# Performance work log

Measured on AMD Instinct MI355X. Metric: run time of the kernel, lower is better.

The kernel has to match this reference:

```python
import jax, jax.numpy as jnp
import numpy as np

B, L, A, D = 4096, 4096, 4, 128


def setup_inputs() -> dict:
    key = jax.random.key(0)
    ks = jax.random.split(key, 12)
    return {
        "sequence": jax.random.randint(ks[0], (B, L), 0, A, dtype=jnp.int32),
        "baseline_sketch": jax.random.normal(ks[1], (B, D), dtype=jnp.float32),
        # learnable params (match torch init distributions)
        "char_scales": 1.0 + 0.2 * jax.random.normal(ks[2], (A,), dtype=jnp.float32),
        "dimension_weights": 1.0 + 0.3 * jax.random.normal(ks[3], (D,), dtype=jnp.float32),
        "sketch_bias": jnp.zeros((D,), dtype=jnp.float32),
        "char_hash_modifiers": 0.1 * jax.random.normal(ks[4], (A, D), dtype=jnp.float32),
        "W1": jax.random.normal(ks[5], (D, D), dtype=jnp.float32) / np.sqrt(D),
        "b1": jnp.zeros((D,), dtype=jnp.float32),
        "W2": jax.random.normal(ks[6], (D, D), dtype=jnp.float32) / np.sqrt(D),
        "b2": jnp.zeros((D,), dtype=jnp.float32),
    }


def _char_counts(sequence, alphabet_size):
    # Fused histogram over the batch: counts[b, a] = #{t : sequence[b, t] == a, 0 <= a < A}
    b, l = sequence.shape
    valid = (sequence >= 0) & (sequence < alphabet_size)
    # out-of-range chars go to an overflow bucket that is dropped
    ids = jnp.where(valid, sequence, alphabet_size) + (
        jnp.arange(b, dtype=sequence.dtype)[:, None] * (alphabet_size + 1)
    )
    counts = jax.ops.segment_sum(
        jnp.ones((b * l,), dtype=jnp.float32),
        ids.reshape(-1),
        num_segments=b * (alphabet_size + 1),
    ).reshape(b, alphabet_size + 1)[:, :alphabet_size]
    return counts  # [B, A]


def reference(sequence, baseline_sketch, char_scales, dimension_weights,
              sketch_bias, char_hash_modifiers, W1, b1, W2, b2):
    l = sequence.shape[1]
    counts = _char_counts(sequence, char_scales.shape[0])          # [B, A]
    char_probs = counts / l                                        # [B, A]
    scale = char_probs @ char_scales                               # [B]
    # scatter-sum of modifier rows == counts @ modifiers
    mods = (counts @ char_hash_modifiers) / l                      # [B, D]
    e = baseline_sketch * dimension_weights + sketch_bias          # [B, D]
    e = e * scale[:, None] + mods                                  # [B, D]
    h = jax.nn.relu(e @ W1.T + b1)                                 # [B, D]
    return h @ W2.T + b2                                           # [B, D]
```

## Files before the change

kernel.cpp:

```cpp
#include <hip/hip_runtime.h>


static constexpr int Lc = 4096;
static constexpr int Ac = 4;
static constexpr int Dc = 128;

static constexpr int HROWS = 2;

__global__ __launch_bounds__(256, 4)
void hist_kernel(const int* __restrict__ seq, float* __restrict__ counts_out)
{
    const int t    = threadIdx.x;
    const int wave = t >> 6;
    const int lane = t & 63;
    const long long r0 = (long long)blockIdx.x * HROWS;

    __shared__ unsigned long long part[HROWS][4];

    unsigned long long c0 = 0ull, c1 = 0ull;
    {
        const int4* p0 = reinterpret_cast<const int4*>(seq + r0 * Lc);
        const int4* p1 = reinterpret_cast<const int4*>(seq + (r0 + 1) * Lc);
        #pragma unroll
        for (int i = 0; i < Lc / 4 / 256; ++i) {
            const int4 a = p0[i * 256 + t];
            const int4 b = p1[i * 256 + t];
            c0 += 1ull << (((unsigned)a.x & 3u) << 4);
            c0 += 1ull << (((unsigned)a.y & 3u) << 4);
            c0 += 1ull << (((unsigned)a.z & 3u) << 4);
            c0 += 1ull << (((unsigned)a.w & 3u) << 4);
            c1 += 1ull << (((unsigned)b.x & 3u) << 4);
            c1 += 1ull << (((unsigned)b.y & 3u) << 4);
            c1 += 1ull << (((unsigned)b.z & 3u) << 4);
            c1 += 1ull << (((unsigned)b.w & 3u) << 4);
        }
    }
    #pragma unroll
    for (int off = 32; off > 0; off >>= 1) {
        c0 += __shfl_down(c0, off);
        c1 += __shfl_down(c1, off);
    }
    if (lane == 0) { part[0][wave] = c0; part[1][wave] = c1; }
    __syncthreads();

    if (t < HROWS * 4) {
        const int rw = t >> 2, a = t & 3;
        const unsigned long long s =
            part[rw][0] + part[rw][1] + part[rw][2] + part[rw][3];
        counts_out[(r0 + rw) * Dc + a] =
            (float)((unsigned)((s >> (a * 16)) & 0xFFFFull));
    }
}

static constexpr int RPB = 8;

__global__ __launch_bounds__(256, 2)
void mlp_kernel(
    const float* __restrict__ baseline,
    const float* __restrict__ char_scales,
    const float* __restrict__ dim_w,
    const float* __restrict__ sk_bias,
    const float* __restrict__ mods,
    const float* __restrict__ W1,
    const float* __restrict__ b1,
    const float* __restrict__ W2,
    const float* __restrict__ b2,
    float*       __restrict__ out)
{
    __shared__ __align__(16) float e_lds[RPB][Dc];
    __shared__ __align__(16) float h_lds[RPB][Dc];
    __shared__ __align__(16) float psum[8][RPB][Dc];

    const int t    = threadIdx.x;
    const int r0   = blockIdx.x * RPB;
    const int j    = t & (Dc - 1);
    const int half = t >> 7;
    const float invL = 1.0f / (float)Lc;

    {
        const float s0 = char_scales[0], s1 = char_scales[1],
                    s2 = char_scales[2], s3 = char_scales[3];
        const float dwj = dim_w[j], bj = sk_bias[j];
        const float m0 = mods[0 * Dc + j], m1 = mods[1 * Dc + j],
                    m2 = mods[2 * Dc + j], m3 = mods[3 * Dc + j];
        #pragma unroll
        for (int rr = 0; rr < RPB / 2; ++rr) {
            const int r = half + rr * 2;
            const float* cp = out + (long long)(r0 + r) * Dc;
            const float c0 = cp[0], c1 = cp[1], c2 = cp[2], c3 = cp[3];
            const float scale = (c0 * s0 + c1 * s1 + c2 * s2 + c3 * s3) * invL;
            const float md    = (c0 * m0 + c1 * m1 + c2 * m2 + c3 * m3) * invL;
            const float base  = baseline[(long long)(r0 + r) * Dc + j];
            e_lds[r][j] = (base * dwj + bj) * scale + md;
        }
    }
    __syncthreads();

    const int q  = t >> 5;
    const int jg = t & 31;
    const int k0 = q * 16;

    {
        float a0[RPB], a1[RPB], a2[RPB], a3[RPB];
        #pragma unroll
        for (int r = 0; r < RPB; ++r) { a0[r] = 0.f; a1[r] = 0.f; a2[r] = 0.f; a3[r] = 0.f; }
        const float4* w0 = reinterpret_cast<const float4*>(W1 + (jg     ) * Dc + k0);
        const float4* w1 = reinterpret_cast<const float4*>(W1 + (jg + 32) * Dc + k0);
        const float4* w2 = reinterpret_cast<const float4*>(W1 + (jg + 64) * Dc + k0);
        const float4* w3 = reinterpret_cast<const float4*>(W1 + (jg + 96) * Dc + k0);
        #pragma unroll
        for (int kk = 0; kk < 4; ++kk) {
            const float4 wa = w0[kk];
            const float4 wb = w1[kk];
            const float4 wc = w2[kk];
            const float4 wd = w3[kk];
            #pragma unroll
            for (int r = 0; r < RPB; ++r) {
                const float4 e = *reinterpret_cast<const float4*>(&e_lds[r][k0 + kk * 4]);
                a0[r] += wa.x * e.x + wa.y * e.y + wa.z * e.z + wa.w * e.w;
                a1[r] += wb.x * e.x + wb.y * e.y + wb.z * e.z + wb.w * e.w;
                a2[r] += wc.x * e.x + wc.y * e.y + wc.z * e.z + wc.w * e.w;
                a3[r] += wd.x * e.x + wd.y * e.y + wd.z * e.z + wd.w * e.w;
            }
        }
        #pragma unroll
        for (int r = 0; r < RPB; ++r) {
            psum[q][r][jg     ] = a0[r];
            psum[q][r][jg + 32] = a1[r];
            psum[q][r][jg + 64] = a2[r];
            psum[q][r][jg + 96] = a3[r];
        }
    }
    __syncthreads();
    {
        const float b = b1[j];
        #pragma unroll
        for (int rr = 0; rr < RPB / 2; ++rr) {
            const int r = half + rr * 2;
            float s = b;
            #pragma unroll
            for (int qq = 0; qq < 8; ++qq) s += psum[qq][r][j];
            h_lds[r][j] = s > 0.0f ? s : 0.0f;
        }
    }
    __syncthreads();

    {
        float a0[RPB], a1[RPB], a2[RPB], a3[RPB];
        #pragma unroll
        for (int r = 0; r < RPB; ++r) { a0[r] = 0.f; a1[r] = 0.f; a2[r] = 0.f; a3[r] = 0.f; }
        const float4* w0 = reinterpret_cast<const float4*>(W2 + (jg     ) * Dc + k0);
        const float4* w1 = reinterpret_cast<const float4*>(W2 + (jg + 32) * Dc + k0);
        const float4* w2 = reinterpret_cast<const float4*>(W2 + (jg + 64) * Dc + k0);
        const float4* w3 = reinterpret_cast<const float4*>(W2 + (jg + 96) * Dc + k0);
        #pragma unroll
        for (int kk = 0; kk < 4; ++kk) {
            const float4 wa = w0[kk];
            const float4 wb = w1[kk];
            const float4 wc = w2[kk];
            const float4 wd = w3[kk];
            #pragma unroll
            for (int r = 0; r < RPB; ++r) {
                const float4 h = *reinterpret_cast<const float4*>(&h_lds[r][k0 + kk * 4]);
                a0[r] += wa.x * h.x + wa.y * h.y + wa.z * h.z + wa.w * h.w;
                a1[r] += wb.x * h.x + wb.y * h.y + wb.z * h.z + wb.w * h.w;
                a2[r] += wc.x * h.x + wc.y * h.y + wc.z * h.z + wc.w * h.w;
                a3[r] += wd.x * h.x + wd.y * h.y + wd.z * h.z + wd.w * h.w;
            }
        }
        #pragma unroll
        for (int r = 0; r < RPB; ++r) {
            psum[q][r][jg     ] = a0[r];
            psum[q][r][jg + 32] = a1[r];
            psum[q][r][jg + 64] = a2[r];
            psum[q][r][jg + 96] = a3[r];
        }
    }
    __syncthreads();
    {
        const float b = b2[j];
        #pragma unroll
        for (int rr = 0; rr < RPB / 2; ++rr) {
            const int r = half + rr * 2;
            float s = b;
            #pragma unroll
            for (int qq = 0; qq < 8; ++qq) s += psum[qq][r][j];
            out[(long long)(r0 + r) * Dc + j] = s;
        }
    }
}

extern "C" void kernel_launch(void* const* d_in, const int* in_sizes, int n_in,
                              void* d_out, int out_size, void* d_ws, size_t ws_size,
                              hipStream_t stream) {
    const int*   seq         = (const int*)  d_in[0];
    const float* baseline    = (const float*)d_in[1];
    const float* char_scales = (const float*)d_in[2];
    const float* dim_w       = (const float*)d_in[3];
    const float* sk_bias     = (const float*)d_in[4];
    const float* mods        = (const float*)d_in[5];
    const float* W1          = (const float*)d_in[6];
    const float* b1          = (const float*)d_in[7];
    const float* W2          = (const float*)d_in[8];
    const float* b2          = (const float*)d_in[9];
    float*       out         = (float*)d_out;

    const int B = in_sizes[1] / Dc;

    hipLaunchKernelGGL(hist_kernel, dim3(B / HROWS), dim3(256), 0, stream,
                       seq, out);
    hipLaunchKernelGGL(mlp_kernel, dim3(B / RPB), dim3(256), 0, stream,
                       baseline, char_scales, dim_w, sk_bias, mods,
                       W1, b1, W2, b2, out);
}
```

Measured before the change: 117.0 us.

## Fuse histogram and MLP into a single kernel with two rows per block

After: 134.3 us. 14.9% more time.

```diff
diff --git a/kernel.cpp b/kernel.cpp
--- a/kernel.cpp
+++ b/kernel.cpp
@@ -4,58 +4,18 @@
 static constexpr int Lc = 4096;
 static constexpr int Ac = 4;
 static constexpr int Dc = 128;
-
-static constexpr int HROWS = 2;
+static constexpr int RPB = 2;
+
+static __device__ __forceinline__ unsigned long long expand8to16(unsigned c) {
+    return  (unsigned long long)(c         & 0xFFu)
+         | ((unsigned long long)((c >>  8) & 0xFFu) << 16)
+         | ((unsigned long long)((c >> 16) & 0xFFu) << 32)
+         | ((unsigned long long)( c >> 24        ) << 48);
+}
 
 __global__ __launch_bounds__(256, 4)
-void hist_kernel(const int* __restrict__ seq, float* __restrict__ counts_out)
-{
-    const int t    = threadIdx.x;
-    const int wave = t >> 6;
-    const int lane = t & 63;
-    const long long r0 = (long long)blockIdx.x * HROWS;
-
-    __shared__ unsigned long long part[HROWS][4];
-
-    unsigned long long c0 = 0ull, c1 = 0ull;
-    {
-        const int4* p0 = reinterpret_cast<const int4*>(seq + r0 * Lc);
-        const int4* p1 = reinterpret_cast<const int4*>(seq + (r0 + 1) * Lc);
-        #pragma unroll
-        for (int i = 0; i < Lc / 4 / 256; ++i) {
-            const int4 a = p0[i * 256 + t];
-            const int4 b = p1[i * 256 + t];
-            c0 += 1ull << (((unsigned)a.x & 3u) << 4);
-            c0 += 1ull << (((unsigned)a.y & 3u) << 4);
-            c0 += 1ull << (((unsigned)a.z & 3u) << 4);
-            c0 += 1ull << (((unsigned)a.w & 3u) << 4);
-            c1 += 1ull << (((unsigned)b.x & 3u) << 4);
-            c1 += 1ull << (((unsigned)b.y & 3u) << 4);
-            c1 += 1ull << (((unsigned)b.z & 3u) << 4);
-            c1 += 1ull << (((unsigned)b.w & 3u) << 4);
-        }
-    }
-    #pragma unroll
-    for (int off = 32; off > 0; off >>= 1) {
-        c0 += __shfl_down(c0, off);
-        c1 += __shfl_down(c1, off);
-    }
-    if (lane == 0) { part[0][wave] = c0; part[1][wave] = c1; }
-    __syncthreads();
-
-    if (t < HROWS * 4) {
-        const int rw = t >> 2, a = t & 3;
-        const unsigned long long s =
-            part[rw][0] + part[rw][1] + part[rw][2] + part[rw][3];
-        counts_out[(r0 + rw) * Dc + a] =
-            (float)((unsigned)((s >> (a * 16)) & 0xFFFFull));
-    }
-}
-
-static constexpr int RPB = 8;
-
-__global__ __launch_bounds__(256, 2)
-void mlp_kernel(
+void fused_sketch_kernel(
+    const int*   __restrict__ seq,
     const float* __restrict__ baseline,
     const float* __restrict__ char_scales,
     const float* __restrict__ dim_w,
@@ -67,12 +27,52 @@
     const float* __restrict__ b2,
     float*       __restrict__ out)
 {
+    __shared__ unsigned long long part[RPB][4];
+    __shared__ float counts_lds[RPB][Ac];
     __shared__ __align__(16) float e_lds[RPB][Dc];
     __shared__ __align__(16) float h_lds[RPB][Dc];
     __shared__ __align__(16) float psum[8][RPB][Dc];
 
     const int t    = threadIdx.x;
-    const int r0   = blockIdx.x * RPB;
+    const int wave = t >> 6;
+    const int lane = t & 63;
+    const long long r0 = (long long)blockIdx.x * RPB;
+
+    {
+        const int4* p0 = reinterpret_cast<const int4*>(seq + r0 * Lc);
+        const int4* p1 = reinterpret_cast<const int4*>(seq + (r0 + 1) * Lc);
+        unsigned c0 = 0u, c1 = 0u;
+        #pragma unroll
+        for (int i = 0; i < Lc / 4 / 256; ++i) {
+            const int4 a = p0[i * 256 + t];
+            const int4 b = p1[i * 256 + t];
+            c0 += 1u << (((unsigned)a.x & 3u) << 3);
+            c0 += 1u << (((unsigned)a.y & 3u) << 3);
+            c0 += 1u << (((unsigned)a.z & 3u) << 3);
+            c0 += 1u << (((unsigned)a.w & 3u) << 3);
+            c1 += 1u << (((unsigned)b.x & 3u) << 3);
+            c1 += 1u << (((unsigned)b.y & 3u) << 3);
+            c1 += 1u << (((unsigned)b.z & 3u) << 3);
+            c1 += 1u << (((unsigned)b.w & 3u) << 3);
+        }
+        unsigned long long w0 = expand8to16(c0);
+        unsigned long long w1 = expand8to16(c1);
+        #pragma unroll
+        for (int off = 32; off > 0; off >>= 1) {
+            w0 += __shfl_down(w0, off);
+            w1 += __shfl_down(w1, off);
+        }
+        if (lane == 0) { part[0][wave] = w0; part[1][wave] = w1; }
+    }
+    __syncthreads();
+    if (t < RPB * 4) {
+        const int rw = t >> 2, a = t & 3;
+        const unsigned long long s =
+            part[rw][0] + part[rw][1] + part[rw][2] + part[rw][3];
+        counts_lds[rw][a] = (float)((unsigned)((s >> (a * 16)) & 0xFFFFull));
+    }
+    __syncthreads();
+
     const int j    = t & (Dc - 1);
     const int half = t >> 7;
     const float invL = 1.0f / (float)Lc;
@@ -83,16 +83,13 @@
         const float dwj = dim_w[j], bj = sk_bias[j];
         const float m0 = mods[0 * Dc + j], m1 = mods[1 * Dc + j],
                     m2 = mods[2 * Dc + j], m3 = mods[3 * Dc + j];
-        #pragma unroll
-        for (int rr = 0; rr < RPB / 2; ++rr) {
-            const int r = half + rr * 2;
-            const float* cp = out + (long long)(r0 + r) * Dc;
-            const float c0 = cp[0], c1 = cp[1], c2 = cp[2], c3 = cp[3];
-            const float scale = (c0 * s0 + c1 * s1 + c2 * s2 + c3 * s3) * invL;
-            const float md    = (c0 * m0 + c1 * m1 + c2 * m2 + c3 * m3) * invL;
-            const float base  = baseline[(long long)(r0 + r) * Dc + j];
-            e_lds[r][j] = (base * dwj + bj) * scale + md;
-        }
+        const int r = half;
+        const float c0 = counts_lds[r][0], c1 = counts_lds[r][1],
+                    c2 = counts_lds[r][2], c3 = counts_lds[r][3];
+        const float scale = (c0 * s0 + c1 * s1 + c2 * s2 + c3 * s3) * invL;
+        const float md    = (c0 * m0 + c1 * m1 + c2 * m2 + c3 * m3) * invL;
+        const float base  = baseline[(r0 + r) * Dc + j];
+        e_lds[r][j] = (base * dwj + bj) * scale + md;
     }
     __syncthreads();
 
@@ -133,15 +130,11 @@
     }
     __syncthreads();
     {
-        const float b = b1[j];
-        #pragma unroll
-        for (int rr = 0; rr < RPB / 2; ++rr) {
-            const int r = half + rr * 2;
-            float s = b;
-            #pragma unroll
-            for (int qq = 0; qq < 8; ++qq) s += psum[qq][r][j];
-            h_lds[r][j] = s > 0.0f ? s : 0.0f;
-        }
+        const int r = half;
+        float s = b1[j];
+        #pragma unroll
+        for (int qq = 0; qq < 8; ++qq) s += psum[qq][r][j];
+        h_lds[r][j] = s > 0.0f ? s : 0.0f;
     }
     __syncthreads();
 
@@ -178,15 +171,11 @@
     }
     __syncthreads();
     {
-        const float b = b2[j];
-        #pragma unroll
-        for (int rr = 0; rr < RPB / 2; ++rr) {
-            const int r = half + rr * 2;
-            float s = b;
-            #pragma unroll
-            for (int qq = 0; qq < 8; ++qq) s += psum[qq][r][j];
-            out[(long long)(r0 + r) * Dc + j] = s;
-        }
+        const int r = half;
+        float s = b2[j];
+        #pragma unroll
+        for (int qq = 0; qq < 8; ++qq) s += psum[qq][r][j];
+        out[(r0 + r) * Dc + j] = s;
     }
 }
 
@@ -206,10 +195,7 @@
     float*       out         = (float*)d_out;
 
     const int B = in_sizes[1] / Dc;
-
-    hipLaunchKernelGGL(hist_kernel, dim3(B / HROWS), dim3(256), 0, stream,
-                       seq, out);
-    hipLaunchKernelGGL(mlp_kernel, dim3(B / RPB), dim3(256), 0, stream,
-                       baseline, char_scales, dim_w, sk_bias, mods,
+    hipLaunchKernelGGL(fused_sketch_kernel, dim3(B / RPB), dim3(256), 0, stream,
+                       seq, baseline, char_scales, dim_w, sk_bias, mods,
                        W1, b1, W2, b2, out);
 }
```
